# Kernel tuning notes

Measured on AMD Instinct MI355X. Metric: run time of the kernel, lower is better.

The kernel has to match this reference:

```python
import jax, jax.numpy as jnp
import numpy as np

N = 100000          # num nodes
NUM_GRAPHS = 64
NEG_SLOPE = 0.2     # PyG GATv2Conv default


def gatv2_layer(x, src, dst, Wl, bl, Wr, br, att, bias, heads, out_ch, concat):
    # x: [N, F_in]; src/dst: [E] (self-loops already included)
    xl = (x @ Wl + bl).reshape(-1, heads, out_ch)   # source transform
    xr = (x @ Wr + br).reshape(-1, heads, out_ch)   # target transform
    m = jax.nn.leaky_relu(xl[src] + xr[dst], NEG_SLOPE)      # [E, H, C]
    alpha = jnp.einsum('ehc,hc->eh', m, att)                 # [E, H]
    # segment softmax over destination nodes
    amax = jax.ops.segment_max(alpha, dst, num_segments=N)
    alpha = jnp.exp(alpha - amax[dst])
    denom = jax.ops.segment_sum(alpha, dst, num_segments=N)
    alpha = alpha / (denom[dst] + 1e-16)
    out = jax.ops.segment_sum(xl[src] * alpha[..., None], dst, num_segments=N)
    out = out.reshape(N, heads * out_ch) if concat else out.mean(axis=1)
    return out + bias


def setup_inputs() -> dict:
    key = jax.random.key(0)
    ks = jax.random.split(key, 16)
    E = 3200000
    x = jax.random.normal(ks[0], (N, 256), dtype=jnp.float32)
    edge_index = jax.random.randint(ks[1], (2, E), 0, N, dtype=jnp.int64)
    batch = jnp.sort(jax.random.randint(ks[2], (N,), 0, NUM_GRAPHS, dtype=jnp.int64))
    H1, C1 = 8, 4
    s1 = 1.0 / np.sqrt(256)
    s2 = 1.0 / np.sqrt(H1 * C1)
    return {
        'x': x, 'edge_index': edge_index, 'batch': batch,
        'W1l': jax.random.normal(ks[3], (256, H1 * C1), jnp.float32) * s1,
        'b1l': jnp.zeros((H1 * C1,), jnp.float32),
        'W1r': jax.random.normal(ks[4], (256, H1 * C1), jnp.float32) * s1,
        'b1r': jnp.zeros((H1 * C1,), jnp.float32),
        'att1': jax.random.normal(ks[5], (H1, C1), jnp.float32),
        'bias1': jnp.zeros((H1 * C1,), jnp.float32),
        'W2l': jax.random.normal(ks[6], (H1 * C1, 64), jnp.float32) * s2,
        'b2l': jnp.zeros((64,), jnp.float32),
        'W2r': jax.random.normal(ks[7], (H1 * C1, 64), jnp.float32) * s2,
        'b2r': jnp.zeros((64,), jnp.float32),
        'att2': jax.random.normal(ks[8], (1, 64), jnp.float32),
        'bias2': jnp.zeros((64,), jnp.float32),
    }


def reference(x, edge_index, batch, W1l, b1l, W1r, b1r, att1, bias1,
              W2l, b2l, W2r, b2r, att2, bias2):
    # add self-loops (PyG GATv2Conv default add_self_loops=True)
    loop = jnp.arange(N, dtype=edge_index.dtype)
    src = jnp.concatenate([edge_index[0], loop])
    dst = jnp.concatenate([edge_index[1], loop])
    h = gatv2_layer(x, src, dst, W1l, b1l, W1r, b1r, att1, bias1, 8, 4, True)
    h = jax.nn.elu(h)
    h = gatv2_layer(h, src, dst, W2l, b2l, W2r, b2r, att2, bias2, 1, 64, False)
    # global mean pool over graphs
    sums = jax.ops.segment_sum(h, batch, num_segments=NUM_GRAPHS)
    counts = jax.ops.segment_sum(jnp.ones((N, 1), h.dtype), batch, num_segments=NUM_GRAPHS)
    return sums / jnp.maximum(counts, 1.0)
```

## Files before the change

### kernel.cpp

```cpp
#include <hip/hip_runtime.h>
#include <math.h>

#define NN 100000
#define EE 3200000
#define ET (EE + NN)
#define NG 64

#define NB 196
#define BWID 512
#define PCHUNK 8192
#define PBLOCKS ((ET + PCHUNK - 1) / PCHUNK)

#define OFF_XL1B  0u
#define OFF_XR1   1600000u
#define OFF_H     4800000u
#define OFF_HL2B  8000000u
#define OFF_HR2   11200000u
#define OFF_BEDGE 8000000u
#define OFF_RP    17600000u
#define OFF_ESRC  17700096u
#define OFF_POOL  21000096u
#define OFF_CNTG  21004192u
#define OFF_BCNT  21004256u
#define OFF_BOFF  21004512u
#define OFF_GCUR  21004768u
#define WS_UNITS  21005024u

__device__ __forceinline__ float lrelu(float v) { return v > 0.0f ? v : 0.2f * v; }

__device__ __forceinline__ unsigned pack_bf2(float a, float b) {
  unsigned ua = __float_as_uint(a), ub = __float_as_uint(b);
  ua = (ua + 0x7FFFu + ((ua >> 16) & 1u)) >> 16;
  ub = (ub + 0x7FFFu + ((ub >> 16) & 1u)) & 0xFFFF0000u;
  return ua | ub;
}
__device__ __forceinline__ float bf_lo(unsigned u) { return __uint_as_float(u << 16); }
__device__ __forceinline__ float bf_hi(unsigned u) { return __uint_as_float(u & 0xFFFF0000u); }

__global__ __launch_bounds__(256) void k_bcount(const int* __restrict__ ei,
                                                int* __restrict__ bcnt) {
  __shared__ int h[NB];
  for (int i = threadIdx.x; i < NB; i += 256) h[i] = 0;
  __syncthreads();
  for (long e = (long)blockIdx.x * 256 + threadIdx.x; e < ET; e += (long)gridDim.x * 256) {
    int d = (e < EE) ? ei[EE + e] : (int)(e - EE);
    atomicAdd(&h[d >> 9], 1);
  }
  __syncthreads();
  for (int i = threadIdx.x; i < NB; i += 256) if (h[i]) atomicAdd(&bcnt[i], h[i]);
}

__global__ __launch_bounds__(256) void k_bscan(const int* __restrict__ bcnt,
                                               int* __restrict__ boff, int* __restrict__ gcur) {
  __shared__ int sd[256];
  int t = threadIdx.x;
  int v = (t < NB) ? bcnt[t] : 0;
  sd[t] = v;
  __syncthreads();
  for (int o = 1; o < 256; o <<= 1) {
    int u = (t >= o) ? sd[t - o] : 0;
    __syncthreads();
    sd[t] += u;
    __syncthreads();
  }
  if (t < NB) { boff[t] = sd[t] - v; gcur[t] = sd[t] - v; }
  if (t == 0) boff[NB] = ET;
}

__global__ __launch_bounds__(512) void k_part(const int* __restrict__ ei,
                                              int* __restrict__ gcur,
                                              int2* __restrict__ bedge) {
  __shared__ int  cnt[NB];
  __shared__ int  lbase[NB];
  __shared__ int  gbase[NB];
  __shared__ int  sc[256];
  __shared__ int2 buf[PCHUNK];
  int tid = threadIdx.x;
  long e0 = (long)blockIdx.x * PCHUNK;
  int nedge = (e0 + PCHUNK <= ET) ? PCHUNK : (int)(ET - e0);

  for (int i = tid; i < NB; i += 512) cnt[i] = 0;
  __syncthreads();
  for (int i = tid; i < nedge; i += 512) {
    long e = e0 + i;
    int d = (e < EE) ? ei[EE + e] : (int)(e - EE);
    atomicAdd(&cnt[d >> 9], 1);
  }
  __syncthreads();
  if (tid < 256) sc[tid] = (tid < NB) ? cnt[tid] : 0;
  __syncthreads();
  for (int o = 1; o < 256; o <<= 1) {
    int u = (tid < 256 && tid >= o) ? sc[tid - o] : 0;
    __syncthreads();
    if (tid < 256) sc[tid] += u;
    __syncthreads();
  }
  if (tid < NB) lbase[tid] = sc[tid] - cnt[tid];
  __syncthreads();
  if (tid < NB) {
    int c = cnt[tid];
    gbase[tid] = c ? atomicAdd(&gcur[tid], c) : 0;
    cnt[tid] = 0;
  }
  __syncthreads();
  for (int i = tid; i < nedge; i += 512) {
    long e = e0 + i;
    int s, d;
    if (e < EE) { s = ei[e]; d = ei[EE + e]; }
    else { s = (int)(e - EE); d = s; }
    int b = d >> 9;
    int r = atomicAdd(&cnt[b], 1);
    buf[lbase[b] + r] = make_int2(s, d);
  }
  __syncthreads();
  for (int i = tid; i < nedge; i += 512) {
    int2 ed = buf[i];
    int b = ed.y >> 9;
    bedge[gbase[b] + (i - lbase[b])] = ed;
  }
}

__global__ __launch_bounds__(512) void k_csr(const int* __restrict__ boff,
                                             const int2* __restrict__ bedge,
                                             int* __restrict__ rp, int* __restrict__ esrc) {
  __shared__ int sdeg[BWID];
  __shared__ int sscan[BWID];
  int b = blockIdx.x, t = threadIdx.x;
  int n0 = b * BWID;
  int lo = boff[b], hi = boff[b + 1];
  sdeg[t] = 0;
  __syncthreads();
  for (int i = lo + t; i < hi; i += 512) {
    int2 ed = bedge[i];
    atomicAdd(&sdeg[ed.y - n0], 1);
  }
  __syncthreads();
  int v = sdeg[t];
  sscan[t] = v;
  __syncthreads();
  for (int o = 1; o < 512; o <<= 1) {
    int u = (t >= o) ? sscan[t - o] : 0;
    __syncthreads();
    sscan[t] += u;
    __syncthreads();
  }
  int excl = sscan[t] - v;
  int n = n0 + t;
  if (n < NN) rp[n] = lo + excl;
  if (b == NB - 1 && t == 0) rp[NN] = ET;
  __syncthreads();
  sdeg[t] = lo + excl;
  __syncthreads();
  for (int i = lo + t; i < hi; i += 512) {
    int2 ed = bedge[i];
    int p = atomicAdd(&sdeg[ed.y - n0], 1);
    esrc[p] = ed.x;
  }
}

#define FMA4A(a, xv) \
  a.x += xv.x*w0.x + xv.y*w1.x + xv.z*w2.x + xv.w*w3.x; \
  a.y += xv.x*w0.y + xv.y*w1.y + xv.z*w2.y + xv.w*w3.y; \
  a.z += xv.x*w0.z + xv.y*w1.z + xv.z*w2.z + xv.w*w3.z; \
  a.w += xv.x*w0.w + xv.y*w1.w + xv.z*w2.w + xv.w*w3.w;

__global__ __launch_bounds__(256) void k_xform1(
    const float* __restrict__ x,
    const float* __restrict__ Wl, const float* __restrict__ bl,
    const float* __restrict__ Wr, const float* __restrict__ br,
    unsigned short* __restrict__ xl1b, float* __restrict__ xr1) {
  __shared__ float Wlds[128 * 64];
  int tid = threadIdx.x;
  int ci = tid & 15, ni = tid >> 4;
  int cbase = ci * 4;
  int n0 = blockIdx.x * 128 + ni * 8;
  const float* xb[8];
#pragma unroll
  for (int j = 0; j < 8; ++j) {
    int r = n0 + j < NN ? n0 + j : NN - 1;
    xb[j] = x + (size_t)r * 256;
  }
  float4 acc[8];
#pragma unroll
  for (int j = 0; j < 8; ++j) acc[j] = make_float4(0.f, 0.f, 0.f, 0.f);

  for (int half = 0; half < 2; ++half) {
    int k0 = half * 128;
    __syncthreads();
    for (int i = tid; i < 128 * 64; i += 256) {
      int k = (i >> 6) + k0, c = i & 63;
      Wlds[i] = (c < 32) ? Wl[k * 32 + c] : Wr[k * 32 + (c - 32)];
    }
    __syncthreads();
    for (int kk = 0; kk < 128; kk += 4) {
      int k = k0 + kk;
      float4 xv[8];
#pragma unroll
      for (int j = 0; j < 8; ++j) xv[j] = *(const float4*)(xb[j] + k);
      const float* wr = &Wlds[kk * 64 + cbase];
      float4 w0 = *(const float4*)(wr);
      float4 w1 = *(const float4*)(wr + 64);
      float4 w2 = *(const float4*)(wr + 128);
      float4 w3 = *(const float4*)(wr + 192);
#pragma unroll
      for (int j = 0; j < 8; ++j) { FMA4A(acc[j], xv[j]) }
    }
  }
  if (cbase < 32) {
    float4 bv = { bl[cbase], bl[cbase+1], bl[cbase+2], bl[cbase+3] };
#pragma unroll
    for (int j = 0; j < 8; ++j) {
      int n = n0 + j;
      if (n < NN) {
        uint2 o = { pack_bf2(acc[j].x + bv.x, acc[j].y + bv.y),
                    pack_bf2(acc[j].z + bv.z, acc[j].w + bv.w) };
        *(uint2*)(xl1b + (size_t)n * 32 + cbase) = o;
      }
    }
  } else {
    int c2 = cbase - 32;
    float4 bv = { br[c2], br[c2+1], br[c2+2], br[c2+3] };
#pragma unroll
    for (int j = 0; j < 8; ++j) {
      int n = n0 + j;
      if (n < NN) {
        float4 o = { acc[j].x + bv.x, acc[j].y + bv.y, acc[j].z + bv.z, acc[j].w + bv.w };
        *(float4*)(xr1 + (size_t)n * 32 + c2) = o;
      }
    }
  }
}

__global__ __launch_bounds__(256) void k_gather1(
    const int* __restrict__ rp, const int* __restrict__ esrc,
    const unsigned short* __restrict__ xl1b, const float* __restrict__ xr1,
    const float* __restrict__ att1, const float* __restrict__ bias1,
    float* __restrict__ h) {
  int n = blockIdx.x * 8 + (threadIdx.x >> 5);
  if (n >= NN) return;
  int l = threadIdx.x & 31;
  float av = att1[l];
  float xr = xr1[(size_t)n * 32 + l];
  int rpn = rp[n], dg = rp[n + 1] - rpn;
  float acc = 0.0f, den = 0.0f;
  int j = 0;
  for (; j + 4 <= dg; j += 4) {
    int s0 = esrc[rpn + j + 0];
    int s1 = esrc[rpn + j + 1];
    int s2 = esrc[rpn + j + 2];
    int s3 = esrc[rpn + j + 3];
    float x0 = bf_lo(xl1b[(size_t)s0 * 32 + l]);
    float x1 = bf_lo(xl1b[(size_t)s1 * 32 + l]);
    float x2 = bf_lo(xl1b[(size_t)s2 * 32 + l]);
    float x3 = bf_lo(xl1b[(size_t)s3 * 32 + l]);
    float p0 = lrelu(x0 + xr) * av;
    float p1 = lrelu(x1 + xr) * av;
    float p2 = lrelu(x2 + xr) * av;
    float p3 = lrelu(x3 + xr) * av;
    p0 += __shfl_xor(p0, 1); p1 += __shfl_xor(p1, 1);
    p2 += __shfl_xor(p2, 1); p3 += __shfl_xor(p3, 1);
    p0 += __shfl_xor(p0, 2); p1 += __shfl_xor(p1, 2);
    p2 += __shfl_xor(p2, 2); p3 += __shfl_xor(p3, 2);
    float w0 = __expf(p0), w1 = __expf(p1), w2 = __expf(p2), w3 = __expf(p3);
    den += w0 + w1 + w2 + w3;
    acc += w0 * x0 + w1 * x1 + w2 * x2 + w3 * x3;
  }
  for (; j < dg; ++j) {
    int s = esrc[rpn + j];
    float xl = bf_lo(xl1b[(size_t)s * 32 + l]);
    float p = lrelu(xl + xr) * av;
    p += __shfl_xor(p, 1);
    p += __shfl_xor(p, 2);
    float w = __expf(p);
    den += w;
    acc += w * xl;
  }
  float v = acc / (den + 1e-16f) + bias1[l];
  h[(size_t)n * 32 + l] = v > 0.0f ? v : expm1f(v);
}

__global__ __launch_bounds__(256) void k_xform2(
    const float* __restrict__ h,
    const float* __restrict__ Wl, const float* __restrict__ bl,
    const float* __restrict__ Wr, const float* __restrict__ br,
    unsigned short* __restrict__ hl2b, float* __restrict__ hr2) {
  __shared__ float Wlds[32 * 128];
  int tid = threadIdx.x;
  for (int i = tid; i < 32 * 128; i += 256) {
    int k = i >> 7, c = i & 127;
    Wlds[i] = (c < 64) ? Wl[k * 64 + c] : Wr[k * 64 + (c - 64)];
  }
  __syncthreads();
  int ci = tid & 31, ni = tid >> 5;
  int cbase = ci * 4;
  int n0 = blockIdx.x * 32 + ni * 4;
  const float* hb0 = h + (size_t)(n0 + 0) * 32;
  const float* hb1 = h + (size_t)(n0 + 1) * 32;
  const float* hb2 = h + (size_t)(n0 + 2) * 32;
  const float* hb3 = h + (size_t)(n0 + 3) * 32;
  float4 acc0 = {0,0,0,0}, acc1 = {0,0,0,0}, acc2 = {0,0,0,0}, acc3 = {0,0,0,0};
#pragma unroll
  for (int k = 0; k < 32; k += 4) {
    float4 xv0 = *(const float4*)(hb0 + k);
    float4 xv1 = *(const float4*)(hb1 + k);
    float4 xv2 = *(const float4*)(hb2 + k);
    float4 xv3 = *(const float4*)(hb3 + k);
    const float* wr = &Wlds[k * 128 + cbase];
    float4 w0 = *(const float4*)(wr);
    float4 w1 = *(const float4*)(wr + 128);
    float4 w2 = *(const float4*)(wr + 256);
    float4 w3 = *(const float4*)(wr + 384);
    FMA4A(acc0, xv0)
    FMA4A(acc1, xv1)
    FMA4A(acc2, xv2)
    FMA4A(acc3, xv3)
  }
  float4 acc[4] = {acc0, acc1, acc2, acc3};
  if (cbase < 64) {
    float4 bv = { bl[cbase], bl[cbase+1], bl[cbase+2], bl[cbase+3] };
#pragma unroll
    for (int j = 0; j < 4; ++j) {
      uint2 o = { pack_bf2(acc[j].x + bv.x, acc[j].y + bv.y),
                  pack_bf2(acc[j].z + bv.z, acc[j].w + bv.w) };
      *(uint2*)(hl2b + (size_t)(n0 + j) * 64 + cbase) = o;
    }
  } else {
    int c2 = cbase - 64;
    float4 bv = { br[c2], br[c2+1], br[c2+2], br[c2+3] };
#pragma unroll
    for (int j = 0; j < 4; ++j) {
      float4 o = { acc[j].x + bv.x, acc[j].y + bv.y, acc[j].z + bv.z, acc[j].w + bv.w };
      *(float4*)(hr2 + (size_t)(n0 + j) * 64 + c2) = o;
    }
  }
}

__global__ __launch_bounds__(256) void k_gather2(
    const int* __restrict__ rp, const int* __restrict__ esrc,
    const unsigned short* __restrict__ hl2b, const float* __restrict__ hr2,
    const float* __restrict__ att2, const float* __restrict__ bias2,
    const int* __restrict__ batch,
    float* __restrict__ pool, float* __restrict__ cntg) {
  __shared__ float ssum[4][64];
  __shared__ float scnt[4];
  int tid = threadIdx.x;
  int n = (blockIdx.x * 256 + tid) >> 3;
  int l8 = tid & 7;
  int nblk0 = blockIdx.x * 32;
  int gmin = batch[nblk0];
  int gspan = batch[nblk0 + 31] - gmin + 1;
  ssum[tid >> 6][tid & 63] = 0.0f;
  if (tid < 4) scnt[tid] = 0.0f;
  __syncthreads();

  float4 ac0 = *(const float4*)(att2 + l8 * 8);
  float4 ac1 = *(const float4*)(att2 + l8 * 8 + 4);
  float4 bs0 = *(const float4*)(bias2 + l8 * 8);
  float4 bs1 = *(const float4*)(bias2 + l8 * 8 + 4);
  const float4* hrp = (const float4*)(hr2 + (size_t)n * 64 + l8 * 8);
  float4 hr0 = hrp[0], hr1 = hrp[1];
  int rpn = rp[n], dg = rp[n + 1] - rpn;
  float4 a0 = {0,0,0,0}, a1 = {0,0,0,0};
  float den = 0.0f;
  int j = 0;
  for (; j + 2 <= dg; j += 2) {
    int s0 = esrc[rpn + j];
    int s1 = esrc[rpn + j + 1];
    uint4 q0 = *(const uint4*)(hl2b + (size_t)s0 * 64 + l8 * 8);
    uint4 q1 = *(const uint4*)(hl2b + (size_t)s1 * 64 + l8 * 8);
    float4 u0 = { bf_lo(q0.x), bf_hi(q0.x), bf_lo(q0.y), bf_hi(q0.y) };
    float4 u1 = { bf_lo(q0.z), bf_hi(q0.z), bf_lo(q0.w), bf_hi(q0.w) };
    float4 v0 = { bf_lo(q1.x), bf_hi(q1.x), bf_lo(q1.y), bf_hi(q1.y) };
    float4 v1 = { bf_lo(q1.z), bf_hi(q1.z), bf_lo(q1.w), bf_hi(q1.w) };
    float p0 = lrelu(u0.x + hr0.x) * ac0.x + lrelu(u0.y + hr0.y) * ac0.y
             + lrelu(u0.z + hr0.z) * ac0.z + lrelu(u0.w + hr0.w) * ac0.w
             + lrelu(u1.x + hr1.x) * ac1.x + lrelu(u1.y + hr1.y) * ac1.y
             + lrelu(u1.z + hr1.z) * ac1.z + lrelu(u1.w + hr1.w) * ac1.w;
    float p1 = lrelu(v0.x + hr0.x) * ac0.x + lrelu(v0.y + hr0.y) * ac0.y
             + lrelu(v0.z + hr0.z) * ac0.z + lrelu(v0.w + hr0.w) * ac0.w
             + lrelu(v1.x + hr1.x) * ac1.x + lrelu(v1.y + hr1.y) * ac1.y
             + lrelu(v1.z + hr1.z) * ac1.z + lrelu(v1.w + hr1.w) * ac1.w;
    p0 += __shfl_xor(p0, 1); p1 += __shfl_xor(p1, 1);
    p0 += __shfl_xor(p0, 2); p1 += __shfl_xor(p1, 2);
    p0 += __shfl_xor(p0, 4); p1 += __shfl_xor(p1, 4);
    float w0 = __expf(p0), w1 = __expf(p1);
    den += w0 + w1;
    a0.x += w0 * u0.x + w1 * v0.x; a0.y += w0 * u0.y + w1 * v0.y;
    a0.z += w0 * u0.z + w1 * v0.z; a0.w += w0 * u0.w + w1 * v0.w;
    a1.x += w0 * u1.x + w1 * v1.x; a1.y += w0 * u1.y + w1 * v1.y;
    a1.z += w0 * u1.z + w1 * v1.z; a1.w += w0 * u1.w + w1 * v1.w;
  }
  for (; j < dg; ++j) {
    int s = esrc[rpn + j];
    uint4 q0 = *(const uint4*)(hl2b + (size_t)s * 64 + l8 * 8);
    float4 u0 = { bf_lo(q0.x), bf_hi(q0.x), bf_lo(q0.y), bf_hi(q0.y) };
    float4 u1 = { bf_lo(q0.z), bf_hi(q0.z), bf_lo(q0.w), bf_hi(q0.w) };
    float p = lrelu(u0.x + hr0.x) * ac0.x + lrelu(u0.y + hr0.y) * ac0.y
            + lrelu(u0.z + hr0.z) * ac0.z + lrelu(u0.w + hr0.w) * ac0.w
            + lrelu(u1.x + hr1.x) * ac1.x + lrelu(u1.y + hr1.y) * ac1.y
            + lrelu(u1.z + hr1.z) * ac1.z + lrelu(u1.w + hr1.w) * ac1.w;
    p += __shfl_xor(p, 1);
    p += __shfl_xor(p, 2);
    p += __shfl_xor(p, 4);
    float w = __expf(p);
    den += w;
    a0.x += w * u0.x; a0.y += w * u0.y; a0.z += w * u0.z; a0.w += w * u0.w;
    a1.x += w * u1.x; a1.y += w * u1.y; a1.z += w * u1.z; a1.w += w * u1.w;
  }
  float inv = 1.0f / (den + 1e-16f);
  int gi = batch[n] - gmin;
  float* sp = &ssum[gi][l8 * 8];
  atomicAdd(sp + 0, a0.x * inv + bs0.x);
  atomicAdd(sp + 1, a0.y * inv + bs0.y);
  atomicAdd(sp + 2, a0.z * inv + bs0.z);
  atomicAdd(sp + 3, a0.w * inv + bs0.w);
  atomicAdd(sp + 4, a1.x * inv + bs1.x);
  atomicAdd(sp + 5, a1.y * inv + bs1.y);
  atomicAdd(sp + 6, a1.z * inv + bs1.z);
  atomicAdd(sp + 7, a1.w * inv + bs1.w);
  if (l8 == 0) atomicAdd(&scnt[gi], 1.0f);
  __syncthreads();
  for (int i = tid; i < gspan * 64; i += 256)
    atomicAdd(pool + (size_t)(gmin + (i >> 6)) * 64 + (i & 63), ssum[i >> 6][i & 63]);
  if (tid < gspan) atomicAdd(cntg + gmin + tid, scnt[tid]);
}

__global__ __launch_bounds__(256) void k_final(
    const float* __restrict__ pool, const float* __restrict__ cntg,
    float* __restrict__ out) {
  int i = blockIdx.x * 256 + threadIdx.x;
  if (i < NG * 64) out[i] = pool[i] / fmaxf(cntg[i >> 6], 1.0f);
}

extern "C" void kernel_launch(void* const* d_in, const int* in_sizes, int n_in,
                              void* d_out, int out_size, void* d_ws, size_t ws_size,
                              hipStream_t stream) {
  const float* x     = (const float*)d_in[0];
  const int*   ei    = (const int*)d_in[1];
  const int*   batch = (const int*)d_in[2];
  const float* W1l   = (const float*)d_in[3];
  const float* b1l   = (const float*)d_in[4];
  const float* W1r   = (const float*)d_in[5];
  const float* b1r   = (const float*)d_in[6];
  const float* att1  = (const float*)d_in[7];
  const float* bias1 = (const float*)d_in[8];
  const float* W2l   = (const float*)d_in[9];
  const float* b2l   = (const float*)d_in[10];
  const float* W2r   = (const float*)d_in[11];
  const float* b2r   = (const float*)d_in[12];
  const float* att2  = (const float*)d_in[13];
  const float* bias2 = (const float*)d_in[14];
  float* ws = (float*)d_ws;
  int*   wi = (int*)d_ws;
  float* out = (float*)d_out;

  hipMemsetAsync(ws + OFF_POOL, 0, (size_t)(WS_UNITS - OFF_POOL) * 4, stream);

  k_bcount<<<512, 256, 0, stream>>>(ei, wi + OFF_BCNT);
  k_bscan<<<1, 256, 0, stream>>>(wi + OFF_BCNT, wi + OFF_BOFF, wi + OFF_GCUR);
  k_part<<<PBLOCKS, 512, 0, stream>>>(ei, wi + OFF_GCUR, (int2*)(wi + OFF_BEDGE));
  k_csr<<<NB, 512, 0, stream>>>(wi + OFF_BOFF, (const int2*)(wi + OFF_BEDGE),
                                wi + OFF_RP, wi + OFF_ESRC);

  k_xform1<<<(NN + 127) / 128, 256, 0, stream>>>(x, W1l, b1l, W1r, b1r,
                                                 (unsigned short*)(ws + OFF_XL1B), ws + OFF_XR1);
  k_gather1<<<NN / 8, 256, 0, stream>>>(wi + OFF_RP, wi + OFF_ESRC,
                                        (const unsigned short*)(ws + OFF_XL1B), ws + OFF_XR1,
                                        att1, bias1, ws + OFF_H);
  k_xform2<<<NN / 32, 256, 0, stream>>>(ws + OFF_H, W2l, b2l, W2r, b2r,
                                        (unsigned short*)(ws + OFF_HL2B), ws + OFF_HR2);
  k_gather2<<<(NN * 8 + 255) / 256, 256, 0, stream>>>(wi + OFF_RP, wi + OFF_ESRC,
                                                      (const unsigned short*)(ws + OFF_HL2B),
                                                      ws + OFF_HR2, att2, bias2, batch,
                                                      ws + OFF_POOL, ws + OFF_CNTG);
  k_final<<<16, 256, 0, stream>>>(ws + OFF_POOL, ws + OFF_CNTG, out);
}
```

Before: 400.4 us.

## Pack bucketed edges into one int and retile the first-layer transform

Edges in the partition buffer are now packed as a single 32-bit word (17-bit source plus a 9-bit local destination offset), with a separate byte array holding the bucket id. This halves the global traffic of the bucketed edge array written by k_part and read twice by k_csr, and shrinks its shared-memory staging. Separately, k_xform1 now processes 64 nodes per block with 4 rows per thread and a smaller weight tile loaded in four quarters, with launch bounds set for higher occupancy. That trades register reuse for more resident waves. The packing relies on node ids fitting in 17 bits.

```diff
diff --git a/kernel.cpp b/kernel.cpp
--- a/kernel.cpp
+++ b/kernel.cpp
@@ -69,12 +69,13 @@
 
 __global__ __launch_bounds__(512) void k_part(const int* __restrict__ ei,
                                               int* __restrict__ gcur,
-                                              int2* __restrict__ bedge) {
+                                              int* __restrict__ bedge) {
   __shared__ int  cnt[NB];
   __shared__ int  lbase[NB];
   __shared__ int  gbase[NB];
   __shared__ int  sc[256];
-  __shared__ int2 buf[PCHUNK];
+  __shared__ int  buf[PCHUNK];
+  __shared__ unsigned char bkt[PCHUNK];
   int tid = threadIdx.x;
   long e0 = (long)blockIdx.x * PCHUNK;
   int nedge = (e0 + PCHUNK <= ET) ? PCHUNK : (int)(ET - e0);
@@ -110,18 +111,20 @@
     else { s = (int)(e - EE); d = s; }
     int b = d >> 9;
     int r = atomicAdd(&cnt[b], 1);
-    buf[lbase[b] + r] = make_int2(s, d);
+    int idx = lbase[b] + r;
+    buf[idx] = s | ((d & 511) << 17);
+    bkt[idx] = (unsigned char)b;
   }
   __syncthreads();
   for (int i = tid; i < nedge; i += 512) {
-    int2 ed = buf[i];
-    int b = ed.y >> 9;
-    bedge[gbase[b] + (i - lbase[b])] = ed;
+    int p = buf[i];
+    int b = bkt[i];
+    bedge[gbase[b] + (i - lbase[b])] = p;
   }
 }
 
 __global__ __launch_bounds__(512) void k_csr(const int* __restrict__ boff,
-                                             const int2* __restrict__ bedge,
+                                             const int* __restrict__ bedge,
                                              int* __restrict__ rp, int* __restrict__ esrc) {
   __shared__ int sdeg[BWID];
   __shared__ int sscan[BWID];
@@ -131,8 +134,8 @@
   sdeg[t] = 0;
   __syncthreads();
   for (int i = lo + t; i < hi; i += 512) {
-    int2 ed = bedge[i];
-    atomicAdd(&sdeg[ed.y - n0], 1);
+    int p = bedge[i];
+    atomicAdd(&sdeg[p >> 17], 1);
   }
   __syncthreads();
   int v = sdeg[t];
@@ -152,9 +155,9 @@
   sdeg[t] = lo + excl;
   __syncthreads();
   for (int i = lo + t; i < hi; i += 512) {
-    int2 ed = bedge[i];
-    int p = atomicAdd(&sdeg[ed.y - n0], 1);
-    esrc[p] = ed.x;
+    int p = bedge[i];
+    int pos = atomicAdd(&sdeg[p >> 17], 1);
+    esrc[pos] = p & 0x1FFFF;
   }
 }
 
@@ -164,52 +167,57 @@
   a.z += xv.x*w0.z + xv.y*w1.z + xv.z*w2.z + xv.w*w3.z; \
   a.w += xv.x*w0.w + xv.y*w1.w + xv.z*w2.w + xv.w*w3.w;
 
-__global__ __launch_bounds__(256) void k_xform1(
+__global__ __launch_bounds__(256, 8) void k_xform1(
     const float* __restrict__ x,
     const float* __restrict__ Wl, const float* __restrict__ bl,
     const float* __restrict__ Wr, const float* __restrict__ br,
     unsigned short* __restrict__ xl1b, float* __restrict__ xr1) {
-  __shared__ float Wlds[128 * 64];
+  __shared__ float Wlds[64 * 64];
   int tid = threadIdx.x;
   int ci = tid & 15, ni = tid >> 4;
   int cbase = ci * 4;
-  int n0 = blockIdx.x * 128 + ni * 8;
-  const float* xb[8];
-#pragma unroll
-  for (int j = 0; j < 8; ++j) {
-    int r = n0 + j < NN ? n0 + j : NN - 1;
-    xb[j] = x + (size_t)r * 256;
-  }
-  float4 acc[8];
-#pragma unroll
-  for (int j = 0; j < 8; ++j) acc[j] = make_float4(0.f, 0.f, 0.f, 0.f);
-
-  for (int half = 0; half < 2; ++half) {
-    int k0 = half * 128;
-    __syncthreads();
-    for (int i = tid; i < 128 * 64; i += 256) {
+  int n0 = blockIdx.x * 64 + ni * 4;
+  int r0 = n0 + 0 < NN ? n0 + 0 : NN - 1;
+  int r1 = n0 + 1 < NN ? n0 + 1 : NN - 1;
+  int r2 = n0 + 2 < NN ? n0 + 2 : NN - 1;
+  int r3 = n0 + 3 < NN ? n0 + 3 : NN - 1;
+  const float* xb0 = x + (size_t)r0 * 256;
+  const float* xb1 = x + (size_t)r1 * 256;
+  const float* xb2 = x + (size_t)r2 * 256;
+  const float* xb3 = x + (size_t)r3 * 256;
+  float4 acc0 = {0,0,0,0}, acc1 = {0,0,0,0}, acc2 = {0,0,0,0}, acc3 = {0,0,0,0};
+
+  for (int q = 0; q < 4; ++q) {
+    int k0 = q * 64;
+    __syncthreads();
+    for (int i = tid; i < 64 * 64; i += 256) {
       int k = (i >> 6) + k0, c = i & 63;
       Wlds[i] = (c < 32) ? Wl[k * 32 + c] : Wr[k * 32 + (c - 32)];
     }
     __syncthreads();
-    for (int kk = 0; kk < 128; kk += 4) {
+#pragma unroll 2
+    for (int kk = 0; kk < 64; kk += 4) {
       int k = k0 + kk;
-      float4 xv[8];
-#pragma unroll
-      for (int j = 0; j < 8; ++j) xv[j] = *(const float4*)(xb[j] + k);
+      float4 xv0 = *(const float4*)(xb0 + k);
+      float4 xv1 = *(const float4*)(xb1 + k);
+      float4 xv2 = *(const float4*)(xb2 + k);
+      float4 xv3 = *(const float4*)(xb3 + k);
       const float* wr = &Wlds[kk * 64 + cbase];
       float4 w0 = *(const float4*)(wr);
       float4 w1 = *(const float4*)(wr + 64);
       float4 w2 = *(const float4*)(wr + 128);
       float4 w3 = *(const float4*)(wr + 192);
-#pragma unroll
-      for (int j = 0; j < 8; ++j) { FMA4A(acc[j], xv[j]) }
-    }
-  }
+      FMA4A(acc0, xv0)
+      FMA4A(acc1, xv1)
+      FMA4A(acc2, xv2)
+      FMA4A(acc3, xv3)
+    }
+  }
+  float4 acc[4] = {acc0, acc1, acc2, acc3};
   if (cbase < 32) {
     float4 bv = { bl[cbase], bl[cbase+1], bl[cbase+2], bl[cbase+3] };
 #pragma unroll
-    for (int j = 0; j < 8; ++j) {
+    for (int j = 0; j < 4; ++j) {
       int n = n0 + j;
       if (n < NN) {
         uint2 o = { pack_bf2(acc[j].x + bv.x, acc[j].y + bv.y),
@@ -221,7 +229,7 @@
     int c2 = cbase - 32;
     float4 bv = { br[c2], br[c2+1], br[c2+2], br[c2+3] };
 #pragma unroll
-    for (int j = 0; j < 8; ++j) {
+    for (int j = 0; j < 4; ++j) {
       int n = n0 + j;
       if (n < NN) {
         float4 o = { acc[j].x + bv.x, acc[j].y + bv.y, acc[j].z + bv.z, acc[j].w + bv.w };
@@ -458,12 +466,12 @@
 
   k_bcount<<<512, 256, 0, stream>>>(ei, wi + OFF_BCNT);
   k_bscan<<<1, 256, 0, stream>>>(wi + OFF_BCNT, wi + OFF_BOFF, wi + OFF_GCUR);
-  k_part<<<PBLOCKS, 512, 0, stream>>>(ei, wi + OFF_GCUR, (int2*)(wi + OFF_BEDGE));
-  k_csr<<<NB, 512, 0, stream>>>(wi + OFF_BOFF, (const int2*)(wi + OFF_BEDGE),
+  k_part<<<PBLOCKS, 512, 0, stream>>>(ei, wi + OFF_GCUR, wi + OFF_BEDGE);
+  k_csr<<<NB, 512, 0, stream>>>(wi + OFF_BOFF, wi + OFF_BEDGE,
                                 wi + OFF_RP, wi + OFF_ESRC);
 
-  k_xform1<<<(NN + 127) / 128, 256, 0, stream>>>(x, W1l, b1l, W1r, b1r,
-                                                 (unsigned short*)(ws + OFF_XL1B), ws + OFF_XR1);
+  k_xform1<<<(NN + 63) / 64, 256, 0, stream>>>(x, W1l, b1l, W1r, b1r,
+                                               (unsigned short*)(ws + OFF_XL1B), ws + OFF_XR1);
   k_gather1<<<NN / 8, 256, 0, stream>>>(wi + OFF_RP, wi + OFF_ESRC,
                                         (const unsigned short*)(ws + OFF_XL1B), ws + OFF_XR1,
                                         att1, bias1, ws + OFF_H);
```

Measured after the change: 559.2 us. 39.6% more time.
